# Performance work log

Hardware: AMD Instinct MI355X
Metric: run time of the kernel (lower is better)

The kernel has to match this reference:

```python
import jax, jax.numpy as jnp
import numpy as np

ALPHA = 0.25
GAMMA = 2.0
OBJ_POS_WEIGHT = 1.5
CLS_W, REG_W, OBJ_W = 2.5, 5.0, 0.5
B, M, C, IMG = 64, 50, 4, 1280


def setup_inputs() -> dict:
    key = jax.random.key(0)
    ks = jax.random.split(key, 12)
    shapes = {
        'cls_p3': (B, C, 160, 160), 'reg_p3': (B, 4, 160, 160), 'obj_p3': (B, 1, 160, 160),
        'cls_p4': (B, C, 80, 80),   'reg_p4': (B, 4, 80, 80),   'obj_p4': (B, 1, 80, 80),
        'cls_p5': (B, C, 40, 40),   'reg_p5': (B, 4, 40, 40),   'obj_p5': (B, 1, 40, 40),
    }
    inp = {name: jax.random.normal(k, s, dtype=jnp.float32)
           for (name, s), k in zip(shapes.items(), ks[:9])}
    # boxes in pixel xyxy: sample two corners uniformly, sort so x2>=x1, y2>=y1
    raw = jax.random.uniform(ks[9], (B, M, 4), dtype=jnp.float32) * IMG
    x1 = jnp.minimum(raw[..., 0], raw[..., 2]); x2 = jnp.maximum(raw[..., 0], raw[..., 2])
    y1 = jnp.minimum(raw[..., 1], raw[..., 3]); y2 = jnp.maximum(raw[..., 1], raw[..., 3])
    inp['boxes'] = jnp.stack([x1, y1, x2, y2], axis=-1)
    inp['labels'] = jax.random.randint(ks[10], (B, M), 0, C, dtype=jnp.int32)
    inp['box_valid'] = jax.random.randint(ks[11], (B, M), 0, 2, dtype=jnp.int32)
    inp['img_size'] = IMG
    return inp


def _bce_logits(x, t):
    # numerically stable BCE-with-logits, elementwise
    return jnp.maximum(x, 0.0) - x * t + jnp.log1p(jnp.exp(-jnp.abs(x)))


def _focal(x, t):
    bce = _bce_logits(x, t)
    p = jax.nn.sigmoid(x)
    p_t = p * t + (1.0 - p) * (1.0 - t)
    a_w = ALPHA * t + (1.0 - ALPHA) * (1.0 - t)
    return jnp.mean(a_w * (1.0 - p_t) ** GAMMA * bce)


def _smooth_l1(d):
    a = jnp.abs(d)
    return jnp.where(a < 1.0, 0.5 * d * d, a - 0.5)


def _build_targets(boxes, labels, valid, stride, Bn, Cn, H, W):
    cx = (boxes[..., 0] + boxes[..., 2]) * 0.5 / stride  # [B,M]
    cy = (boxes[..., 1] + boxes[..., 3]) * 0.5 / stride
    gx = jnp.clip(cx.astype(jnp.int32), 0, W - 1)
    gy = jnp.clip(cy.astype(jnp.int32), 0, H - 1)
    gy_s = jnp.where(valid > 0, gy, H)  # invalid boxes -> out of bounds -> dropped
    b = jnp.broadcast_to(jnp.arange(Bn)[:, None], gx.shape)
    w = jnp.maximum(boxes[..., 2] - boxes[..., 0], 1.0)
    h = jnp.maximum(boxes[..., 3] - boxes[..., 1], 1.0)
    vals = jnp.stack([cx - gx.astype(cx.dtype), cy - gy.astype(cy.dtype),
                      jnp.log(w / stride), jnp.log(h / stride)], axis=-1)  # [B,M,4]
    cls_t = jnp.zeros((Bn, Cn, H, W), jnp.float32).at[b, labels, gy_s, gx].set(1.0, mode='drop')
    obj_t = jnp.zeros((Bn, 1, H, W), jnp.float32).at[b, 0, gy_s, gx].set(1.0, mode='drop')
    ch = jnp.arange(4)
    reg_t = jnp.zeros((Bn, 4, H, W), jnp.float32).at[
        b[:, :, None], ch[None, None, :], gy_s[:, :, None], gx[:, :, None]].set(vals, mode='drop')
    mask = jnp.zeros((Bn, 1, H, W), jnp.float32).at[b, 0, gy_s, gx].set(1.0, mode='drop')
    return cls_t, reg_t, obj_t, mask


def _detection_loss(scales, boxes, labels, valid):
    total_cls = jnp.float32(0.0); total_reg = jnp.float32(0.0); total_obj = jnp.float32(0.0)
    for (cls_p, reg_p, obj_p, stride) in scales:
        Bn, Cn, H, W = cls_p.shape
        cls_t, reg_t, obj_t, mask = _build_targets(boxes, labels, valid, stride, Bn, Cn, H, W)
        total_cls = total_cls + _focal(cls_p, cls_t)
        # BCEWithLogits with pos_weight on positives, mean reduction
        obj_bce = -(OBJ_POS_WEIGHT * obj_t * jax.nn.log_sigmoid(obj_p)
                    + (1.0 - obj_t) * jax.nn.log_sigmoid(-obj_p))
        total_obj = total_obj + jnp.mean(obj_bce)
        mask4 = jnp.broadcast_to(mask, reg_p.shape)
        denom = jnp.sum(mask4)
        reg_l = jnp.sum(_smooth_l1(reg_p - reg_t) * mask4) / jnp.maximum(denom, 1.0)
        total_reg = total_reg + jnp.where(denom > 0, reg_l, 0.0)
    total = CLS_W * total_cls + REG_W * total_reg + OBJ_W * total_obj
    return total, total_cls, total_reg, total_obj


def reference(cls_p3, reg_p3, obj_p3, cls_p4, reg_p4, obj_p4, cls_p5, reg_p5, obj_p5,
              boxes, labels, box_valid, img_size):
    scales = [(cls_p3, reg_p3, obj_p3, 8.0),
              (cls_p4, reg_p4, obj_p4, 16.0),
              (cls_p5, reg_p5, obj_p5, 32.0)]
    return _detection_loss(scales, boxes, labels, box_valid)
```

## Files before the change

### kernel.cpp

```cpp
#include <hip/hip_runtime.h>
#include <math.h>

static constexpr int Bn = 64, Mn = 50, Cn = 4;
static constexpr int TOTAL_BLOCKS = 525;

static constexpr int BASE_OFF = 12 * 64;

#define LOG2E 1.4426950408889634f
#define LN2   0.6931471805599453f

__device__ __forceinline__ float frcp (float x){ return __builtin_amdgcn_rcpf(x); }
__device__ __forceinline__ float fexp2(float x){ return __builtin_amdgcn_exp2f(x); }
__device__ __forceinline__ float flog2(float x){ return __builtin_amdgcn_logf(x); }

__device__ __forceinline__ float proc4(float4 v, float cf) {
  float s = 0.f;
  const float* px = &v.x;
#pragma unroll
  for (int k = 0; k < 4; ++k) {
    float x = px[k];
    float e   = fexp2(-LOG2E * fabsf(x));
    float ope = 1.f + e;
    float u   = frcp(ope);
    float sp  = fmaxf(x, 0.f) + LN2 * flog2(ope);
    float p   = (x >= 0.f) ? u : (1.f - u);
    float w   = fmaf(cf, fmaf(0.75f, p * p, -1.f), 1.f);
    s = fmaf(sp, w, s);
  }
  return s;
}

__device__ __forceinline__ float wave_reduce(float v) {
#pragma unroll
  for (int off = 32; off > 0; off >>= 1) v += __shfl_down(v, off, 64);
  return v;
}

__global__ __launch_bounds__(1024, 8) void main_kernel(
    const float* __restrict__ cls3, const float* __restrict__ reg3, const float* __restrict__ obj3,
    const float* __restrict__ cls4, const float* __restrict__ reg4, const float* __restrict__ obj4,
    const float* __restrict__ cls5, const float* __restrict__ reg5, const float* __restrict__ obj5,
    const float* __restrict__ boxes, const int* __restrict__ labels, const int* __restrict__ valid,
    float* __restrict__ ws) {
  __shared__ float sdata[16];
  const int bid = blockIdx.x;
  const int tid = threadIdx.x;

  const float4* sb; int lb; float cf;
  if (bid < 320)      { sb = (const float4*)cls3; lb = bid;       cf = 1.f; }
  else if (bid < 400) { sb = (const float4*)cls4; lb = bid - 320; cf = 1.f; }
  else if (bid < 420) { sb = (const float4*)cls5; lb = bid - 400; cf = 1.f; }
  else if (bid < 500) { sb = (const float4*)obj3; lb = bid - 420; cf = 0.f; }
  else if (bid < 520) { sb = (const float4*)obj4; lb = bid - 500; cf = 0.f; }
  else                { sb = (const float4*)obj5; lb = bid - 520; cf = 0.f; }

  const float4* p = sb + (size_t)lb * 5120 + tid;
  float4 v0 = p[0];
  float4 v1 = p[1024];
  float4 v2 = p[2048];
  float4 v3 = p[3072];
  float4 v4 = p[4096];

  if (bid < 64) {
    __shared__ int s_cell[3][Mn];
    __shared__ int s_lab[Mn];
    __shared__ float cacc[12];

    const int b = bid;
    if (tid < 12) cacc[tid] = 0.f;

    const int s = tid / Mn;
    const int m = tid - s * Mn;

    float x1 = 0.f, y1 = 0.f, x2 = 0.f, y2 = 0.f;
    int lab = 0, val = 0;
    float cx = 0.f, cy = 0.f, strf = 8.f;
    int gx = 0, gy = 0, cell = -1, W = 160;

    if (tid < 150) {
      const float* bp = boxes + ((size_t)b * Mn + m) * 4;
      x1 = bp[0]; y1 = bp[1]; x2 = bp[2]; y2 = bp[3];
      lab = labels[b * Mn + m];
      val = valid[b * Mn + m];
      if (s == 0) s_lab[m] = lab;

      W = 160 >> s;
      strf = (float)(8 << s);
      if (val > 0) {
        float inv_s = frcp(strf);
        cx = (x1 + x2) * 0.5f * inv_s;
        cy = (y1 + y2) * 0.5f * inv_s;
        gx = min(max((int)cx, 0), W - 1);
        gy = min(max((int)cy, 0), W - 1);
        cell = gy * W + gx;
      }
      s_cell[s][m] = cell;
    }
    __syncthreads();

    if (tid < 150 && cell >= 0) {
      const float* clsP = (s == 0) ? cls3 : ((s == 1) ? cls4 : cls5);
      const float* regP = (s == 0) ? reg3 : ((s == 1) ? reg4 : reg5);
      const float* objP = (s == 0) ? obj3 : ((s == 1) ? obj4 : obj5);

      bool firstObj = true, lastReg = true, firstCls = true;
      for (int j = 0; j < Mn; ++j) {
        if (j == m) continue;
        if (s_cell[s][j] != cell) continue;
        if (j < m) {
          firstObj = false;
          if (s_lab[j] == lab) firstCls = false;
        } else {
          lastReg = false;
        }
      }
      size_t plane = (size_t)W * W;
      size_t pix = (size_t)gy * W + gx;

      if (firstObj) {
        float x = objP[(size_t)b * plane + pix];
        float e = fexp2(-LOG2E * fabsf(x));
        float sp = fmaxf(x, 0.f) + LN2 * flog2(1.f + e);
        float corr = 0.5f * sp - 1.5f * x;
        atomicAdd(&cacc[3 + s], corr);
        atomicAdd(&cacc[9 + s], 4.0f);
      }
      if (firstCls) {
        float x = clsP[((size_t)b * Cn + lab) * plane + pix];
        float e = fexp2(-LOG2E * fabsf(x));
        float ope = 1.f + e;
        float u = frcp(ope);
        float sp = fmaxf(x, 0.f) + LN2 * flog2(ope);
        float spn = sp - x;
        float p2 = (x >= 0.f) ? u : (1.f - u);
        float q = 1.f - p2;
        float corr = 0.25f * q * q * spn - 0.75f * p2 * p2 * sp;
        atomicAdd(&cacc[0 + s], corr);
      }
      if (lastReg) {
        float w = fmaxf(x2 - x1, 1.f), h = fmaxf(y2 - y1, 1.f);
        float inv_s = frcp(strf);
        float t0 = cx - (float)gx, t1 = cy - (float)gy;
        float t2 = LN2 * flog2(w * inv_s), t3 = LN2 * flog2(h * inv_s);
        const float* rp = regP + (size_t)b * 4 * plane + pix;
        float sum = 0.f, dd, a;
        dd = rp[0]         - t0; a = fabsf(dd); sum += (a < 1.f) ? 0.5f * dd * dd : a - 0.5f;
        dd = rp[plane]     - t1; a = fabsf(dd); sum += (a < 1.f) ? 0.5f * dd * dd : a - 0.5f;
        dd = rp[2 * plane] - t2; a = fabsf(dd); sum += (a < 1.f) ? 0.5f * dd * dd : a - 0.5f;
        dd = rp[3 * plane] - t3; a = fabsf(dd); sum += (a < 1.f) ? 0.5f * dd * dd : a - 0.5f;
        atomicAdd(&cacc[6 + s], sum);
      }
    }
    __syncthreads();
    if (tid < 12) ws[tid * 64 + b] = cacc[tid];
  }

  float s = proc4(v0, cf) + proc4(v1, cf) + proc4(v2, cf)
          + proc4(v3, cf) + proc4(v4, cf);

  s = wave_reduce(s);
  const int lane = tid & 63;
  const int wid = tid >> 6;
  if (lane == 0) sdata[wid] = s;
  __syncthreads();
  if (tid == 0) {
    float r = 0.f;
#pragma unroll
    for (int i = 0; i < 16; ++i) r += sdata[i];
    ws[BASE_OFF + bid] = r;
  }
}

__global__ __launch_bounds__(256) void finalize_kernel(
    const float* __restrict__ ws, float* __restrict__ out) {
  __shared__ float sdata[6][4];
  __shared__ float res[18];
  const int t = threadIdx.x;
  const int lane = t & 63;
  const int wid = t >> 6;

  float a0 = 0.f, a1 = 0.f, a2 = 0.f, a3 = 0.f, a4 = 0.f, a5 = 0.f;
  for (int i = t; i < TOTAL_BLOCKS; i += 256) {
    float v = ws[BASE_OFF + i];
    if (i < 320)      a0 += v;
    else if (i < 400) a1 += v;
    else if (i < 420) a2 += v;
    else if (i < 500) a3 += v;
    else if (i < 520) a4 += v;
    else              a5 += v;
  }
  float acc[6] = {a0, a1, a2, a3, a4, a5};
#pragma unroll
  for (int k = 0; k < 6; ++k) {
    float s = wave_reduce(acc[k]);
    if (lane == 0) sdata[k][wid] = s;
  }
  __syncthreads();
  if (t < 6) res[t] = sdata[t][0] + sdata[t][1] + sdata[t][2] + sdata[t][3];

  if (wid == 0) {
#pragma unroll
    for (int j = 0; j < 12; ++j) {
      float v = ws[j * 64 + lane];
      v = wave_reduce(v);
      if (lane == 0) res[6 + j] = v;
    }
  }
  __syncthreads();

  if (t == 0) {
    const float cls_cnt[3] = {6553600.f, 1638400.f, 409600.f};
    const float obj_cnt[3] = {1638400.f, 409600.f, 102400.f};
    float tc = 0.f, to = 0.f, tr = 0.f;
#pragma unroll
    for (int s = 0; s < 3; ++s) {
      tc += (res[s] + res[6 + s]) / cls_cnt[s];
      to += (res[3 + s] + res[9 + s]) / obj_cnt[s];
      float den = res[15 + s];
      if (den > 0.f) tr += res[12 + s] / fmaxf(den, 1.f);
    }
    float total = 2.5f * tc + 5.0f * tr + 0.5f * to;
    out[0] = total; out[1] = tc; out[2] = tr; out[3] = to;
  }
}

extern "C" void kernel_launch(void* const* d_in, const int* in_sizes, int n_in,
                              void* d_out, int out_size, void* d_ws, size_t ws_size,
                              hipStream_t stream) {
  const float* cls3 = (const float*)d_in[0];
  const float* reg3 = (const float*)d_in[1];
  const float* obj3 = (const float*)d_in[2];
  const float* cls4 = (const float*)d_in[3];
  const float* reg4 = (const float*)d_in[4];
  const float* obj4 = (const float*)d_in[5];
  const float* cls5 = (const float*)d_in[6];
  const float* reg5 = (const float*)d_in[7];
  const float* obj5 = (const float*)d_in[8];
  const float* boxes = (const float*)d_in[9];
  const int* labels = (const int*)d_in[10];
  const int* valid = (const int*)d_in[11];
  float* ws = (float*)d_ws;
  float* out = (float*)d_out;

  main_kernel<<<TOTAL_BLOCKS, 1024, 0, stream>>>(
      cls3, reg3, obj3, cls4, reg4, obj4, cls5, reg5, obj5,
      boxes, labels, valid, ws);

  finalize_kernel<<<1, 256, 0, stream>>>(ws, out);
}
```

Before: 25.83 us.

## Split correction work into dedicated blocks and shrink dense blocks to 256 threads

```diff
diff --git a/kernel.cpp b/kernel.cpp
--- a/kernel.cpp
+++ b/kernel.cpp
@@ -2,7 +2,9 @@
 #include <math.h>
 
 static constexpr int Bn = 64, Mn = 50, Cn = 4;
-static constexpr int TOTAL_BLOCKS = 525;
+static constexpr int CORR_BLOCKS = 64;
+static constexpr int DENSE_BLOCKS = 2100;
+static constexpr int TOTAL_BLOCKS = CORR_BLOCKS + DENSE_BLOCKS;
 
 static constexpr int BASE_OFF = 12 * 64;
 
@@ -36,37 +38,20 @@
   return v;
 }
 
-__global__ __launch_bounds__(1024, 8) void main_kernel(
+__global__ __launch_bounds__(256, 8) void main_kernel(
     const float* __restrict__ cls3, const float* __restrict__ reg3, const float* __restrict__ obj3,
     const float* __restrict__ cls4, const float* __restrict__ reg4, const float* __restrict__ obj4,
     const float* __restrict__ cls5, const float* __restrict__ reg5, const float* __restrict__ obj5,
     const float* __restrict__ boxes, const int* __restrict__ labels, const int* __restrict__ valid,
     float* __restrict__ ws) {
-  __shared__ float sdata[16];
-  const int bid = blockIdx.x;
   const int tid = threadIdx.x;
 
-  const float4* sb; int lb; float cf;
-  if (bid < 320)      { sb = (const float4*)cls3; lb = bid;       cf = 1.f; }
-  else if (bid < 400) { sb = (const float4*)cls4; lb = bid - 320; cf = 1.f; }
-  else if (bid < 420) { sb = (const float4*)cls5; lb = bid - 400; cf = 1.f; }
-  else if (bid < 500) { sb = (const float4*)obj3; lb = bid - 420; cf = 0.f; }
-  else if (bid < 520) { sb = (const float4*)obj4; lb = bid - 500; cf = 0.f; }
-  else                { sb = (const float4*)obj5; lb = bid - 520; cf = 0.f; }
-
-  const float4* p = sb + (size_t)lb * 5120 + tid;
-  float4 v0 = p[0];
-  float4 v1 = p[1024];
-  float4 v2 = p[2048];
-  float4 v3 = p[3072];
-  float4 v4 = p[4096];
-
-  if (bid < 64) {
+  if (blockIdx.x < CORR_BLOCKS) {
     __shared__ int s_cell[3][Mn];
     __shared__ int s_lab[Mn];
     __shared__ float cacc[12];
 
-    const int b = bid;
+    const int b = blockIdx.x;
     if (tid < 12) cacc[tid] = 0.f;
 
     const int s = tid / Mn;
@@ -153,21 +138,35 @@
     }
     __syncthreads();
     if (tid < 12) ws[tid * 64 + b] = cacc[tid];
-  }
-
-  float s = proc4(v0, cf) + proc4(v1, cf) + proc4(v2, cf)
-          + proc4(v3, cf) + proc4(v4, cf);
-
-  s = wave_reduce(s);
-  const int lane = tid & 63;
-  const int wid = tid >> 6;
-  if (lane == 0) sdata[wid] = s;
-  __syncthreads();
-  if (tid == 0) {
-    float r = 0.f;
-#pragma unroll
-    for (int i = 0; i < 16; ++i) r += sdata[i];
-    ws[BASE_OFF + bid] = r;
+  } else {
+    __shared__ float sdata[4];
+    const int d = (int)blockIdx.x - CORR_BLOCKS;
+
+    const float4* sb; int lb; float cf;
+    if (d < 1280)      { sb = (const float4*)cls3; lb = d;        cf = 1.f; }
+    else if (d < 1600) { sb = (const float4*)cls4; lb = d - 1280; cf = 1.f; }
+    else if (d < 1680) { sb = (const float4*)cls5; lb = d - 1600; cf = 1.f; }
+    else if (d < 2000) { sb = (const float4*)obj3; lb = d - 1680; cf = 0.f; }
+    else if (d < 2080) { sb = (const float4*)obj4; lb = d - 2000; cf = 0.f; }
+    else               { sb = (const float4*)obj5; lb = d - 2080; cf = 0.f; }
+
+    const float4* p = sb + (size_t)lb * 1280 + tid;
+    float4 v0 = p[0];
+    float4 v1 = p[256];
+    float4 v2 = p[512];
+    float4 v3 = p[768];
+    float4 v4 = p[1024];
+
+    float s = proc4(v0, cf) + proc4(v1, cf) + proc4(v2, cf)
+            + proc4(v3, cf) + proc4(v4, cf);
+
+    s = wave_reduce(s);
+    const int lane = tid & 63;
+    const int wid = tid >> 6;
+    if (lane == 0) sdata[wid] = s;
+    __syncthreads();
+    if (tid == 0)
+      ws[BASE_OFF + d] = sdata[0] + sdata[1] + sdata[2] + sdata[3];
   }
 }
 
@@ -180,14 +179,14 @@
   const int wid = t >> 6;
 
   float a0 = 0.f, a1 = 0.f, a2 = 0.f, a3 = 0.f, a4 = 0.f, a5 = 0.f;
-  for (int i = t; i < TOTAL_BLOCKS; i += 256) {
+  for (int i = t; i < DENSE_BLOCKS; i += 256) {
     float v = ws[BASE_OFF + i];
-    if (i < 320)      a0 += v;
-    else if (i < 400) a1 += v;
-    else if (i < 420) a2 += v;
-    else if (i < 500) a3 += v;
-    else if (i < 520) a4 += v;
-    else              a5 += v;
+    if (i < 1280)      a0 += v;
+    else if (i < 1600) a1 += v;
+    else if (i < 1680) a2 += v;
+    else if (i < 2000) a3 += v;
+    else if (i < 2080) a4 += v;
+    else               a5 += v;
   }
   float acc[6] = {a0, a1, a2, a3, a4, a5};
 #pragma unroll
@@ -242,7 +241,7 @@
   float* ws = (float*)d_ws;
   float* out = (float*)d_out;
 
-  main_kernel<<<TOTAL_BLOCKS, 1024, 0, stream>>>(
+  main_kernel<<<TOTAL_BLOCKS, 256, 0, stream>>>(
       cls3, reg3, obj3, cls4, reg4, obj4, cls5, reg5, obj5,
       boxes, labels, valid, ws);
 
```

Result: faster. 23.74 us (-8.1%).
